# Kernel tuning notes

Measured on AMD Instinct MI355X. Metric: run time of the kernel, lower is better.

Reference implementation:

```python
import jax, jax.numpy as jnp
import numpy as np

B, L, D, H, FFN = 4, 2048, 1024, 8, 2048
DH = D // H  # 128

def layer_norm(x, g, b, eps=1e-5):
    m = jnp.mean(x, axis=-1, keepdims=True)
    v = jnp.mean((x - m) ** 2, axis=-1, keepdims=True)
    return (x - m) * jax.lax.rsqrt(v + eps) * g + b

def setup_inputs() -> dict:
    key = jax.random.key(0)
    ks = jax.random.split(key, 12)
    s = 0.02
    return {
        "inputs": jax.random.normal(ks[0], (B, L, D), jnp.float32),
        "Wq": jax.random.normal(ks[1], (D, D), jnp.float32) * s,
        "bq": jnp.zeros((D,), jnp.float32),
        "Wk": jax.random.normal(ks[2], (D, D), jnp.float32) * s,
        "bk": jnp.zeros((D,), jnp.float32),
        "Wv": jax.random.normal(ks[3], (D, D), jnp.float32) * s,
        "bv": jnp.zeros((D,), jnp.float32),
        "Wo": jax.random.normal(ks[4], (D, D), jnp.float32) * s,
        "bo": jnp.zeros((D,), jnp.float32),
        "ln1_g": jnp.ones((D,), jnp.float32),
        "ln1_b": jnp.zeros((D,), jnp.float32),
        "W1": jax.random.normal(ks[5], (FFN, D), jnp.float32) * s,
        "b1": jnp.zeros((FFN,), jnp.float32),
        "W2": jax.random.normal(ks[6], (D, FFN), jnp.float32) * s,
        "b2": jnp.zeros((D,), jnp.float32),
        "ln2_g": jnp.ones((D,), jnp.float32),
        "ln2_b": jnp.zeros((D,), jnp.float32),
    }

def reference(inputs, Wq, bq, Wk, bk, Wv, bv, Wo, bo, ln1_g, ln1_b, W1, b1, W2, b2, ln2_g, ln2_b):
    b, l, d = inputs.shape
    # linear projections then the original's raw row-major view (no head transpose)
    q = (inputs @ Wq.T + bq).reshape(b * H, -1, DH)
    k = (inputs @ Wk.T + bk).reshape(b * H, -1, DH)
    v = (inputs @ Wv.T + bv).reshape(b * H, -1, DH)
    scale = DH ** -0.5  # (2 * (d_k//2))^-0.5 in the original
    atten = jax.nn.softmax(jnp.einsum('bqd,bkd->bqk', q, k) * scale, axis=-1)
    context = jnp.einsum('bqk,bkd->bqd', atten, v).reshape(b, -1, H * DH)
    out = context @ Wo.T + bo
    h = layer_norm(inputs + out, ln1_g, ln1_b)  # residual + LN (dropout=0)
    # PositionwiseFeedForward: 1x1 conv1d == per-token linear
    f = jax.nn.relu(h @ W1.T + b1) @ W2.T + b2
    y = layer_norm(h + f, ln2_g, ln2_b)
    return (y, atten)
```

## Files before the change

### kernel.cpp

```cpp
#include <hip/hip_runtime.h>
#include <stdint.h>

using f32x4  = __attribute__((ext_vector_type(4))) float;
using f32x16 = __attribute__((ext_vector_type(16))) float;
using bf16x8 = __attribute__((ext_vector_type(8))) short;

#define DEV static __device__ __forceinline__

DEV unsigned short f2bf(float f){
  union { float f; unsigned int u; } c; c.f = f;
  unsigned int u = c.u;
  u += 0x7FFFu + ((u >> 16) & 1u);
  return (unsigned short)(u >> 16);
}
DEV float bf2f(unsigned short u){
  union { unsigned int u; float f; } c; c.u = ((unsigned int)u) << 16; return c.f;
}

DEV void gld_lds16(const void* g, void* l){
  __builtin_amdgcn_global_load_lds(
      (const __attribute__((address_space(1))) void*)g,
      (__attribute__((address_space(3))) void*)l, 16, 0, 0);
}

__global__ __launch_bounds__(256) void cvt_f32_bf16(
    const float* __restrict__ in, unsigned short* __restrict__ out, int n){
  for (int i = (blockIdx.x*256 + threadIdx.x)*4; i < n; i += gridDim.x*1024){
    float4 v = *(const float4*)(in + i);
    ushort4 o; o.x=f2bf(v.x); o.y=f2bf(v.y); o.z=f2bf(v.z); o.w=f2bf(v.w);
    *(ushort4*)(out + i) = o;
  }
}

template<bool OUT_BF16, bool RELU, bool HAS_BIAS>
__global__ __launch_bounds__(256, 2)
void gemm_bt(const unsigned short* __restrict__ Ap, const unsigned short* __restrict__ Bp,
             const float* __restrict__ bias, void* __restrict__ Cp, int N, int K)
{
  constexpr int BM = 128, BN = 128, BK = 32;
  __shared__ __align__(16) unsigned short As[BM*BK];
  __shared__ __align__(16) unsigned short Bs[BN*BK];
  const int tid  = threadIdx.x;
  const int lane = tid & 63;
  const int wid  = tid >> 6;
  const int wr   = wid >> 1, wc = wid & 1;
  const int mrow = lane & 15;
  const int krow = lane >> 4;

  const unsigned short* Ab = Ap + (long)blockIdx.y*BM*K;
  const unsigned short* Bb = Bp + (long)blockIdx.x*BN*K;

  f32x4 acc[4][4] = {};

  for (int k0 = 0; k0 < K; k0 += BK){
    #pragma unroll
    for (int it = 0; it < 2; ++it){
      int ci  = it*256 + tid;
      int row = ci >> 2;
      int col = (ci & 3) * 8;
      gld_lds16(Ab + (long)row*K + k0 + col, (char*)As + it*4096 + wid*1024);
    }
    #pragma unroll
    for (int it = 0; it < 2; ++it){
      int ci  = it*256 + tid;
      int row = ci >> 2;
      int col = (ci & 3) * 8;
      gld_lds16(Bb + (long)row*K + k0 + col, (char*)Bs + it*4096 + wid*1024);
    }
    __syncthreads();

    bf16x8 a[4], b[4];
    #pragma unroll
    for (int mi = 0; mi < 4; ++mi)
      a[mi] = *(const bf16x8*)&As[(wr*64 + mi*16 + mrow)*BK + krow*8];
    #pragma unroll
    for (int ni = 0; ni < 4; ++ni)
      b[ni] = *(const bf16x8*)&Bs[(wc*64 + ni*16 + mrow)*BK + krow*8];
    #pragma unroll
    for (int mi = 0; mi < 4; ++mi)
      #pragma unroll
      for (int ni = 0; ni < 4; ++ni)
        acc[mi][ni] = __builtin_amdgcn_mfma_f32_16x16x32_bf16(a[mi], b[ni], acc[mi][ni], 0, 0, 0);
    __syncthreads();
  }

  int row0 = blockIdx.y*BM + wr*64;
  int col0 = blockIdx.x*BN + wc*64;
  #pragma unroll
  for (int mi = 0; mi < 4; ++mi){
    #pragma unroll
    for (int ni = 0; ni < 4; ++ni){
      int col = col0 + ni*16 + mrow;
      float bv = HAS_BIAS ? bias[col] : 0.f;
      #pragma unroll
      for (int r = 0; r < 4; ++r){
        int row = row0 + mi*16 + krow*4 + r;
        float v = acc[mi][ni][r] + bv;
        if (RELU) v = fmaxf(v, 0.f);
        if (OUT_BF16) ((unsigned short*)Cp)[(long)row*N + col] = f2bf(v);
        else          ((float*)Cp)[(long)row*N + col] = v;
      }
    }
  }
}

__global__ __launch_bounds__(256) void transpose_v(
    const unsigned short* __restrict__ V, unsigned short* __restrict__ Vt){
  __shared__ unsigned short t[32][33];
  int g = blockIdx.z;
  int j0 = blockIdx.x*32, e0 = blockIdx.y*32;
  int tx = threadIdx.x, ty = threadIdx.y;
  const unsigned short* Vg = V + (long)g*262144;
  unsigned short* Vtg = Vt + (long)g*262144;
  #pragma unroll
  for (int i = 0; i < 4; ++i)
    t[ty + 8*i][tx] = Vg[(long)(j0 + ty + 8*i)*128 + e0 + tx];
  __syncthreads();
  #pragma unroll
  for (int i = 0; i < 4; ++i)
    Vtg[(long)(e0 + ty + 8*i)*2048 + j0 + tx] = t[tx][ty + 8*i];
}

__global__ __launch_bounds__(512, 2) void attn_fused(
    const unsigned short* __restrict__ Q, const unsigned short* __restrict__ K,
    const unsigned short* __restrict__ Vt, float* __restrict__ P,
    unsigned short* __restrict__ CTX)
{
  __shared__ __align__(16) char lds[131072];
  char* ldsK = lds;
  char* ldsV = lds + 65536;
  const int tid  = threadIdx.x;
  const int lane = tid & 63;
  const int w    = tid >> 6;
  const int l31  = lane & 31;
  const int hi   = lane >> 5;
  const float scale = 0.08838834764831845f;

  const int d  = blockIdx.x;
  const int g  = (d & 7) + 8*(d >> 6);
  const int qb = (d >> 3) & 7;
  const int q0 = qb * 256;

  const char* KbB = (const char*)(K  + (size_t)g*262144);
  const char* VtB = (const char*)(Vt + (size_t)g*262144);
  const unsigned short* Qb = Q + (size_t)g*262144 + (size_t)(q0 + w*32)*128;
  float* Pb = P + (size_t)g*4194304 + (size_t)(q0 + w*32)*2048;

  bf16x8 qf[8];
  #pragma unroll
  for (int kk = 0; kk < 8; ++kk)
    qf[kk] = *(const bf16x8*)((const char*)Qb + (size_t)l31*256 + kk*32 + hi*16);

  auto stageK = [&](int buf, int jt0){
    #pragma unroll
    for (int r = 0; r < 4; ++r){
      int o = r*8192 + tid*16;
      int j = o >> 8, c = o & 255;
      gld_lds16(KbB + (size_t)(jt0 + j)*256 + (c ^ ((j & 15) << 4)),
                ldsK + buf*32768 + o);
    }
  };
  auto stageV = [&](int buf, int jt0){
    #pragma unroll
    for (int r = 0; r < 4; ++r){
      int o = r*8192 + tid*16;
      int e = o >> 8, c = o & 255;
      gld_lds16(VtB + (size_t)e*4096 + jt0*2 + (c ^ ((e & 15) << 4)),
                ldsV + buf*32768 + o);
    }
  };
  auto readK = [&](int buf, int jloc, int kk) -> bf16x8 {
    int row = jloc + l31;
    int col = (kk*32 + hi*16) ^ ((l31 & 15) << 4);
    return *(const bf16x8*)(ldsK + buf*32768 + row*256 + col);
  };
  auto readV = [&](int buf, int jloc, int c16, int t) -> bf16x8 {
    int row = t*32 + l31;
    int col = (jloc*2 + c16*32 + hi*16) ^ ((l31 & 15) << 4);
    return *(const bf16x8*)(ldsV + buf*32768 + row*256 + col);
  };

  int buf = 0;
  stageK(0, 0);
  __syncthreads();
  float lacc = 0.f;
  for (int st = 0; st < 16; ++st){
    if (st < 15) stageK(buf ^ 1, (st + 1) * 128);
    #pragma unroll
    for (int jt = 0; jt < 4; ++jt){
      const int jloc = jt * 32;
      f32x16 s = {};
      #pragma unroll
      for (int kk = 0; kk < 8; ++kk)
        s = __builtin_amdgcn_mfma_f32_32x32x16_bf16(readK(buf, jloc, kk), qf[kk], s, 0, 0, 0);
      #pragma unroll
      for (int r = 0; r < 16; ++r) lacc += __expf(s[r] * scale);
    }
    __syncthreads();
    buf ^= 1;
  }
  lacc += __shfl_xor(lacc, 32, 64);
  const float invl = 1.f / lacc;

  stageK(0, 0); stageV(0, 0);
  __syncthreads();
  f32x16 O[4] = {};
  buf = 0;
  for (int st = 0; st < 16; ++st){
    if (st < 15){ stageK(buf ^ 1, (st + 1) * 128); stageV(buf ^ 1, (st + 1) * 128); }
    #pragma unroll
    for (int jt = 0; jt < 4; ++jt){
      const int jloc  = jt * 32;
      const int jglob = st*128 + jloc;
      f32x16 s = {};
      #pragma unroll
      for (int kk = 0; kk < 8; ++kk)
        s = __builtin_amdgcn_mfma_f32_32x32x16_bf16(readK(buf, jloc, kk), qf[kk], s, 0, 0, 0);
      float p[16];
      #pragma unroll
      for (int r = 0; r < 16; ++r) p[r] = __expf(s[r] * scale) * invl;
      float* prow = Pb + (size_t)l31*2048 + jglob + hi*4;
      *(float4*)(prow)      = make_float4(p[0],  p[1],  p[2],  p[3]);
      *(float4*)(prow + 8)  = make_float4(p[4],  p[5],  p[6],  p[7]);
      *(float4*)(prow + 16) = make_float4(p[8],  p[9],  p[10], p[11]);
      *(float4*)(prow + 24) = make_float4(p[12], p[13], p[14], p[15]);
      unsigned int pk[8];
      #pragma unroll
      for (int i = 0; i < 8; ++i)
        pk[i] = (unsigned int)f2bf(p[2*i]) | ((unsigned int)f2bf(p[2*i+1]) << 16);
      unsigned int r0 = (unsigned int)__shfl_xor((int)(hi ? pk[0] : pk[2]), 32, 64);
      unsigned int r1 = (unsigned int)__shfl_xor((int)(hi ? pk[1] : pk[3]), 32, 64);
      unsigned int r2 = (unsigned int)__shfl_xor((int)(hi ? pk[4] : pk[6]), 32, 64);
      unsigned int r3 = (unsigned int)__shfl_xor((int)(hi ? pk[5] : pk[7]), 32, 64);
      union U { unsigned int u[4]; bf16x8 v; };
      U a0, a1;
      a0.u[0] = hi ? r0    : pk[0];  a0.u[1] = hi ? r1    : pk[1];
      a0.u[2] = hi ? pk[2] : r0;     a0.u[3] = hi ? pk[3] : r1;
      a1.u[0] = hi ? r2    : pk[4];  a1.u[1] = hi ? r3    : pk[5];
      a1.u[2] = hi ? pk[6] : r2;     a1.u[3] = hi ? pk[7] : r3;
      #pragma unroll
      for (int t = 0; t < 4; ++t){
        O[t] = __builtin_amdgcn_mfma_f32_32x32x16_bf16(a0.v, readV(buf, jloc, 0, t), O[t], 0, 0, 0);
        O[t] = __builtin_amdgcn_mfma_f32_32x32x16_bf16(a1.v, readV(buf, jloc, 1, t), O[t], 0, 0, 0);
      }
    }
    __syncthreads();
    buf ^= 1;
  }

  #pragma unroll
  for (int t = 0; t < 4; ++t){
    #pragma unroll
    for (int r = 0; r < 16; ++r){
      int qrow = (r & 3) + 8*(r >> 2) + 4*hi;
      CTX[(size_t)g*262144 + (size_t)(q0 + w*32 + qrow)*128 + t*32 + l31] = f2bf(O[t][r]);
    }
  }
}

DEV float block_sum256(float v, float* red){
  #pragma unroll
  for (int off = 32; off > 0; off >>= 1) v += __shfl_xor(v, off, 64);
  int lane = threadIdx.x & 63, wid = threadIdx.x >> 6;
  if (lane == 0) red[wid] = v;
  __syncthreads();
  return (red[0]+red[1]) + (red[2]+red[3]);
}

template<bool WRITE_F32, bool WRITE_BF>
__global__ __launch_bounds__(256) void ln_residual(
    const float* __restrict__ X, const float* __restrict__ R,
    const float* __restrict__ gamma, const float* __restrict__ beta,
    float* __restrict__ outf, unsigned short* __restrict__ outb){
  __shared__ float red1[4], red2[4];
  long base = (long)blockIdx.x * 1024;
  int tid = threadIdx.x;
  float4 x = *(const float4*)(X + base + tid*4);
  float4 r = *(const float4*)(R + base + tid*4);
  float v[4] = {x.x+r.x, x.y+r.y, x.z+r.z, x.w+r.w};
  float s = (v[0]+v[1]) + (v[2]+v[3]);
  s = block_sum256(s, red1);
  float mean = s * (1.f/1024.f);
  float d[4] = {v[0]-mean, v[1]-mean, v[2]-mean, v[3]-mean};
  float sq = (d[0]*d[0]+d[1]*d[1]) + (d[2]*d[2]+d[3]*d[3]);
  sq = block_sum256(sq, red2);
  float rstd = rsqrtf(sq*(1.f/1024.f) + 1e-5f);
  float4 g4 = *(const float4*)(gamma + tid*4);
  float4 b4 = *(const float4*)(beta  + tid*4);
  float o[4] = { d[0]*rstd*g4.x + b4.x, d[1]*rstd*g4.y + b4.y,
                 d[2]*rstd*g4.z + b4.z, d[3]*rstd*g4.w + b4.w };
  if (WRITE_F32){
    float4 o4; o4.x=o[0]; o4.y=o[1]; o4.z=o[2]; o4.w=o[3];
    *(float4*)(outf + base + tid*4) = o4;
  }
  if (WRITE_BF){
    ushort4 ob; ob.x=f2bf(o[0]); ob.y=f2bf(o[1]); ob.z=f2bf(o[2]); ob.w=f2bf(o[3]);
    *(ushort4*)(outb + base + tid*4) = ob;
  }
}

extern "C" void kernel_launch(void* const* d_in, const int* in_sizes, int n_in,
                              void* d_out, int out_size, void* d_ws, size_t ws_size,
                              hipStream_t stream){
  const float* X   = (const float*)d_in[0];
  const float* Wq  = (const float*)d_in[1];
  const float* bq  = (const float*)d_in[2];
  const float* Wk  = (const float*)d_in[3];
  const float* bk  = (const float*)d_in[4];
  const float* Wv  = (const float*)d_in[5];
  const float* bv  = (const float*)d_in[6];
  const float* Wo  = (const float*)d_in[7];
  const float* bo  = (const float*)d_in[8];
  const float* g1  = (const float*)d_in[9];
  const float* b1n = (const float*)d_in[10];
  const float* W1  = (const float*)d_in[11];
  const float* b1  = (const float*)d_in[12];
  const float* W2  = (const float*)d_in[13];
  const float* b2  = (const float*)d_in[14];
  const float* g2  = (const float*)d_in[15];
  const float* b2n = (const float*)d_in[16];

  const int M = 8192, D = 1024, F = 2048;
  const long YSZ = (long)M * D;
  float* y_out = (float*)d_out;
  float* atten = (float*)d_out + YSZ;

  char* w = (char*)d_ws;
  auto alloc = [&](size_t bytes){ char* p = w; w += (bytes + 255) & ~(size_t)255; return p; };
  unsigned short* Xbf   = (unsigned short*)alloc((size_t)M*D*2);
  unsigned short* Wqbf  = (unsigned short*)alloc((size_t)D*D*2);
  unsigned short* Wkbf  = (unsigned short*)alloc((size_t)D*D*2);
  unsigned short* Wvbf  = (unsigned short*)alloc((size_t)D*D*2);
  unsigned short* Wobf  = (unsigned short*)alloc((size_t)D*D*2);
  unsigned short* W1bf  = (unsigned short*)alloc((size_t)F*D*2);
  unsigned short* W2bf  = (unsigned short*)alloc((size_t)D*F*2);
  unsigned short* Qbf   = (unsigned short*)alloc((size_t)M*D*2);
  unsigned short* Kbf   = (unsigned short*)alloc((size_t)M*D*2);
  unsigned short* Vbf   = (unsigned short*)alloc((size_t)M*D*2);
  unsigned short* Vtbf  = (unsigned short*)alloc((size_t)M*D*2);
  unsigned short* CTXbf = (unsigned short*)alloc((size_t)M*D*2);
  unsigned short* Hbf   = (unsigned short*)alloc((size_t)M*D*2);
  unsigned short* F1bf  = (unsigned short*)alloc((size_t)M*F*2);
  float*          Hf    = (float*)alloc((size_t)M*D*4);
  float*          TMP   = (float*)alloc((size_t)M*D*4);

  auto cvt = [&](const float* src, unsigned short* dst, int n){
    int blocks = (n/4 + 255)/256; if (blocks > 4096) blocks = 4096;
    cvt_f32_bf16<<<blocks, 256, 0, stream>>>(src, dst, n);
  };
  cvt(X,  Xbf,  M*D);
  cvt(Wq, Wqbf, D*D);  cvt(Wk, Wkbf, D*D);  cvt(Wv, Wvbf, D*D);  cvt(Wo, Wobf, D*D);
  cvt(W1, W1bf, F*D);  cvt(W2, W2bf, D*F);

  dim3 blk(256);

  gemm_bt<true,false,true><<<dim3(D/128, M/128), blk, 0, stream>>>(Xbf, Wqbf, bq, Qbf, D, D);
  gemm_bt<true,false,true><<<dim3(D/128, M/128), blk, 0, stream>>>(Xbf, Wkbf, bk, Kbf, D, D);
  gemm_bt<true,false,true><<<dim3(D/128, M/128), blk, 0, stream>>>(Xbf, Wvbf, bv, Vbf, D, D);

  transpose_v<<<dim3(64, 4, 32), dim3(32, 8), 0, stream>>>(Vbf, Vtbf);

  attn_fused<<<dim3(256), dim3(512), 0, stream>>>(Qbf, Kbf, Vtbf, atten, CTXbf);

  gemm_bt<false,false,true><<<dim3(D/128, M/128), blk, 0, stream>>>(CTXbf, Wobf, bo, TMP, D, D);

  ln_residual<true,true><<<M, 256, 0, stream>>>(X, TMP, g1, b1n, Hf, Hbf);

  gemm_bt<true,true,true><<<dim3(F/128, M/128), blk, 0, stream>>>(Hbf, W1bf, b1, F1bf, F, D);

  gemm_bt<false,false,true><<<dim3(D/128, M/128), blk, 0, stream>>>(F1bf, W2bf, b2, TMP, D, F);

  ln_residual<true,false><<<M, 256, 0, stream>>>(Hf, TMP, g2, b2n, y_out, nullptr);
}
```

Before: 514.7 us.

## Deepen GEMM K tile, prioritize MFMA waves, and carry residuals in bf16

Raises the GEMM K tile to 64 so each barrier pair covers two MFMA k-steps, halving the number of synchronizations per GEMM. Adds s_setprio around the MFMA sections in the attention kernel to favor matrix issue among co-resident waves. Output-projection and FFN2 GEMMs now emit bf16, and the residual+layernorm kernels read bf16 operands (including bf16 X and H), removing the fp32 intermediate buffers. This reduces memory traffic but lowers the residual path's precision, which risks accuracy tolerance.

```diff
diff --git a/kernel.cpp b/kernel.cpp
--- a/kernel.cpp
+++ b/kernel.cpp
@@ -37,7 +37,7 @@
 void gemm_bt(const unsigned short* __restrict__ Ap, const unsigned short* __restrict__ Bp,
              const float* __restrict__ bias, void* __restrict__ Cp, int N, int K)
 {
-  constexpr int BM = 128, BN = 128, BK = 32;
+  constexpr int BM = 128, BN = 128, BK = 64;
   __shared__ __align__(16) unsigned short As[BM*BK];
   __shared__ __align__(16) unsigned short Bs[BN*BK];
   const int tid  = threadIdx.x;
@@ -54,33 +54,36 @@
 
   for (int k0 = 0; k0 < K; k0 += BK){
     #pragma unroll
-    for (int it = 0; it < 2; ++it){
+    for (int it = 0; it < 4; ++it){
       int ci  = it*256 + tid;
-      int row = ci >> 2;
-      int col = (ci & 3) * 8;
+      int row = ci >> 3;
+      int col = (ci & 7) * 8;
       gld_lds16(Ab + (long)row*K + k0 + col, (char*)As + it*4096 + wid*1024);
     }
     #pragma unroll
-    for (int it = 0; it < 2; ++it){
+    for (int it = 0; it < 4; ++it){
       int ci  = it*256 + tid;
-      int row = ci >> 2;
-      int col = (ci & 3) * 8;
+      int row = ci >> 3;
+      int col = (ci & 7) * 8;
       gld_lds16(Bb + (long)row*K + k0 + col, (char*)Bs + it*4096 + wid*1024);
     }
     __syncthreads();
 
-    bf16x8 a[4], b[4];
-    #pragma unroll
-    for (int mi = 0; mi < 4; ++mi)
-      a[mi] = *(const bf16x8*)&As[(wr*64 + mi*16 + mrow)*BK + krow*8];
-    #pragma unroll
-    for (int ni = 0; ni < 4; ++ni)
-      b[ni] = *(const bf16x8*)&Bs[(wc*64 + ni*16 + mrow)*BK + krow*8];
-    #pragma unroll
-    for (int mi = 0; mi < 4; ++mi)
+    #pragma unroll
+    for (int ksub = 0; ksub < 2; ++ksub){
+      bf16x8 a[4], b[4];
+      #pragma unroll
+      for (int mi = 0; mi < 4; ++mi)
+        a[mi] = *(const bf16x8*)&As[(wr*64 + mi*16 + mrow)*BK + ksub*32 + krow*8];
       #pragma unroll
       for (int ni = 0; ni < 4; ++ni)
-        acc[mi][ni] = __builtin_amdgcn_mfma_f32_16x16x32_bf16(a[mi], b[ni], acc[mi][ni], 0, 0, 0);
+        b[ni] = *(const bf16x8*)&Bs[(wc*64 + ni*16 + mrow)*BK + ksub*32 + krow*8];
+      #pragma unroll
+      for (int mi = 0; mi < 4; ++mi)
+        #pragma unroll
+        for (int ni = 0; ni < 4; ++ni)
+          acc[mi][ni] = __builtin_amdgcn_mfma_f32_16x16x32_bf16(a[mi], b[ni], acc[mi][ni], 0, 0, 0);
+    }
     __syncthreads();
   }
 
@@ -190,9 +193,11 @@
     for (int jt = 0; jt < 4; ++jt){
       const int jloc = jt * 32;
       f32x16 s = {};
+      __builtin_amdgcn_s_setprio(1);
       #pragma unroll
       for (int kk = 0; kk < 8; ++kk)
         s = __builtin_amdgcn_mfma_f32_32x32x16_bf16(readK(buf, jloc, kk), qf[kk], s, 0, 0, 0);
+      __builtin_amdgcn_s_setprio(0);
       #pragma unroll
       for (int r = 0; r < 16; ++r) lacc += __expf(s[r] * scale);
     }
@@ -213,21 +218,22 @@
       const int jloc  = jt * 32;
       const int jglob = st*128 + jloc;
       f32x16 s = {};
+      __builtin_amdgcn_s_setprio(1);
       #pragma unroll
       for (int kk = 0; kk < 8; ++kk)
         s = __builtin_amdgcn_mfma_f32_32x32x16_bf16(readK(buf, jloc, kk), qf[kk], s, 0, 0, 0);
-      float p[16];
-      #pragma unroll
-      for (int r = 0; r < 16; ++r) p[r] = __expf(s[r] * scale) * invl;
+      __builtin_amdgcn_s_setprio(0);
+      #pragma unroll
+      for (int r = 0; r < 16; ++r) s[r] = __expf(s[r] * scale) * invl;
       float* prow = Pb + (size_t)l31*2048 + jglob + hi*4;
-      *(float4*)(prow)      = make_float4(p[0],  p[1],  p[2],  p[3]);
-      *(float4*)(prow + 8)  = make_float4(p[4],  p[5],  p[6],  p[7]);
-      *(float4*)(prow + 16) = make_float4(p[8],  p[9],  p[10], p[11]);
-      *(float4*)(prow + 24) = make_float4(p[12], p[13], p[14], p[15]);
+      *(float4*)(prow)      = make_float4(s[0],  s[1],  s[2],  s[3]);
+      *(float4*)(prow + 8)  = make_float4(s[4],  s[5],  s[6],  s[7]);
+      *(float4*)(prow + 16) = make_float4(s[8],  s[9],  s[10], s[11]);
+      *(float4*)(prow + 24) = make_float4(s[12], s[13], s[14], s[15]);
       unsigned int pk[8];
       #pragma unroll
       for (int i = 0; i < 8; ++i)
-        pk[i] = (unsigned int)f2bf(p[2*i]) | ((unsigned int)f2bf(p[2*i+1]) << 16);
+        pk[i] = (unsigned int)f2bf(s[2*i]) | ((unsigned int)f2bf(s[2*i+1]) << 16);
       unsigned int r0 = (unsigned int)__shfl_xor((int)(hi ? pk[0] : pk[2]), 32, 64);
       unsigned int r1 = (unsigned int)__shfl_xor((int)(hi ? pk[1] : pk[3]), 32, 64);
       unsigned int r2 = (unsigned int)__shfl_xor((int)(hi ? pk[4] : pk[6]), 32, 64);
@@ -238,11 +244,13 @@
       a0.u[2] = hi ? pk[2] : r0;     a0.u[3] = hi ? pk[3] : r1;
       a1.u[0] = hi ? r2    : pk[4];  a1.u[1] = hi ? r3    : pk[5];
       a1.u[2] = hi ? pk[6] : r2;     a1.u[3] = hi ? pk[7] : r3;
+      __builtin_amdgcn_s_setprio(1);
       #pragma unroll
       for (int t = 0; t < 4; ++t){
         O[t] = __builtin_amdgcn_mfma_f32_32x32x16_bf16(a0.v, readV(buf, jloc, 0, t), O[t], 0, 0, 0);
         O[t] = __builtin_amdgcn_mfma_f32_32x32x16_bf16(a1.v, readV(buf, jloc, 1, t), O[t], 0, 0, 0);
       }
+      __builtin_amdgcn_s_setprio(0);
     }
     __syncthreads();
     buf ^= 1;
@@ -268,27 +276,28 @@
 }
 
 template<bool WRITE_F32, bool WRITE_BF>
-__global__ __launch_bounds__(256) void ln_residual(
-    const float* __restrict__ X, const float* __restrict__ R,
+__global__ __launch_bounds__(256) void ln_residual_bf(
+    const unsigned short* __restrict__ A, const unsigned short* __restrict__ R,
     const float* __restrict__ gamma, const float* __restrict__ beta,
     float* __restrict__ outf, unsigned short* __restrict__ outb){
   __shared__ float red1[4], red2[4];
   long base = (long)blockIdx.x * 1024;
   int tid = threadIdx.x;
-  float4 x = *(const float4*)(X + base + tid*4);
-  float4 r = *(const float4*)(R + base + tid*4);
-  float v[4] = {x.x+r.x, x.y+r.y, x.z+r.z, x.w+r.w};
+  ushort4 a = *(const ushort4*)(A + base + tid*4);
+  ushort4 r = *(const ushort4*)(R + base + tid*4);
+  float v[4] = { bf2f(a.x)+bf2f(r.x), bf2f(a.y)+bf2f(r.y),
+                 bf2f(a.z)+bf2f(r.z), bf2f(a.w)+bf2f(r.w) };
   float s = (v[0]+v[1]) + (v[2]+v[3]);
   s = block_sum256(s, red1);
   float mean = s * (1.f/1024.f);
-  float d[4] = {v[0]-mean, v[1]-mean, v[2]-mean, v[3]-mean};
-  float sq = (d[0]*d[0]+d[1]*d[1]) + (d[2]*d[2]+d[3]*d[3]);
+  float dd[4] = {v[0]-mean, v[1]-mean, v[2]-mean, v[3]-mean};
+  float sq = (dd[0]*dd[0]+dd[1]*dd[1]) + (dd[2]*dd[2]+dd[3]*dd[3]);
   sq = block_sum256(sq, red2);
   float rstd = rsqrtf(sq*(1.f/1024.f) + 1e-5f);
   float4 g4 = *(const float4*)(gamma + tid*4);
   float4 b4 = *(const float4*)(beta  + tid*4);
-  float o[4] = { d[0]*rstd*g4.x + b4.x, d[1]*rstd*g4.y + b4.y,
-                 d[2]*rstd*g4.z + b4.z, d[3]*rstd*g4.w + b4.w };
+  float o[4] = { dd[0]*rstd*g4.x + b4.x, dd[1]*rstd*g4.y + b4.y,
+                 dd[2]*rstd*g4.z + b4.z, dd[3]*rstd*g4.w + b4.w };
   if (WRITE_F32){
     float4 o4; o4.x=o[0]; o4.y=o[1]; o4.z=o[2]; o4.w=o[3];
     *(float4*)(outf + base + tid*4) = o4;
@@ -341,8 +350,7 @@
   unsigned short* CTXbf = (unsigned short*)alloc((size_t)M*D*2);
   unsigned short* Hbf   = (unsigned short*)alloc((size_t)M*D*2);
   unsigned short* F1bf  = (unsigned short*)alloc((size_t)M*F*2);
-  float*          Hf    = (float*)alloc((size_t)M*D*4);
-  float*          TMP   = (float*)alloc((size_t)M*D*4);
+  unsigned short* TMPbf = (unsigned short*)alloc((size_t)M*D*2);
 
   auto cvt = [&](const float* src, unsigned short* dst, int n){
     int blocks = (n/4 + 255)/256; if (blocks > 4096) blocks = 4096;
@@ -362,13 +370,13 @@
 
   attn_fused<<<dim3(256), dim3(512), 0, stream>>>(Qbf, Kbf, Vtbf, atten, CTXbf);
 
-  gemm_bt<false,false,true><<<dim3(D/128, M/128), blk, 0, stream>>>(CTXbf, Wobf, bo, TMP, D, D);
-
-  ln_residual<true,true><<<M, 256, 0, stream>>>(X, TMP, g1, b1n, Hf, Hbf);
+  gemm_bt<true,false,true><<<dim3(D/128, M/128), blk, 0, stream>>>(CTXbf, Wobf, bo, TMPbf, D, D);
+
+  ln_residual_bf<false,true><<<M, 256, 0, stream>>>(Xbf, TMPbf, g1, b1n, nullptr, Hbf);
 
   gemm_bt<true,true,true><<<dim3(F/128, M/128), blk, 0, stream>>>(Hbf, W1bf, b1, F1bf, F, D);
 
-  gemm_bt<false,false,true><<<dim3(D/128, M/128), blk, 0, stream>>>(F1bf, W2bf, b2, TMP, D, F);
-
-  ln_residual<true,false><<<M, 256, 0, stream>>>(Hf, TMP, g2, b2n, y_out, nullptr);
-}
+  gemm_bt<true,false,true><<<dim3(D/128, M/128), blk, 0, stream>>>(F1bf, W2bf, b2, TMPbf, D, F);
+
+  ln_residual_bf<true,false><<<M, 256, 0, stream>>>(Hbf, TMPbf, g2, b2n, y_out, nullptr);
+}
```

Result: slower. 551.2 us (+7.1%).
